# Performance work log

Hardware: AMD Instinct MI355X
Metric: run time of the kernel (lower is better)

The kernel has to match this reference:

```python
import jax, jax.numpy as jnp
import numpy as np

H = 256   # hid_size
N = 10000 # num vertices
B = 512   # num paths
L = 256   # max path length
E = 64    # max neighbors per last vertex


def _init_params(key):
    ks = jax.random.split(key, 12)
    s = 1.0 / np.sqrt(H)
    u = lambda k, shp: jax.random.uniform(k, shp, jnp.float32, -s, s)
    return dict(
        W_ih=u(ks[0], (4 * H, H)), W_hh=u(ks[1], (4 * H, H)),
        b_ih=u(ks[2], (4 * H,)), b_hh=u(ks[3], (4 * H,)),
        Wa1=u(ks[4], (H, 2 * H)), ba1=u(ks[5], (H,)),
        Wa2=u(ks[6], (1, H)), ba2=u(ks[7], (1,)),
        Wc1=u(ks[8], (H, H)), bc1=u(ks[9], (H,)),
        Wc2=u(ks[10], (1, H)), bc2=u(ks[11], (1,)),
    )


def setup_inputs() -> dict:
    key = jax.random.key(0)
    k = jax.random.split(key, 6)
    inp = dict(
        graph_emb=jax.random.normal(k[0], (N, H), jnp.float32),
        paths=jax.random.randint(k[1], (B, L), 0, N),
        path_lens=jax.random.randint(k[2], (B,), 1, L + 1),
        neighbors=jax.random.randint(k[3], (B, E), 0, N),
        n_neighbors=jax.random.randint(k[4], (B,), 1, E + 1),
    )
    inp.update(_init_params(k[5]))
    return inp


def _forward(graph_emb, paths, path_lens, neighbors, n_neighbors,
             W_ih, W_hh, b_ih, b_hh, Wa1, ba1, Wa2, ba2, Wc1, bc1, Wc2, bc2):
    x = graph_emb[paths]  # [B, L, H] gathered path embeddings
    h0 = jnp.zeros((x.shape[0], W_hh.shape[1]), x.dtype)

    def step(carry, inp):
        h, c = carry
        xt, t = inp  # xt: [B, H]
        gates = xt @ W_ih.T + h @ W_hh.T + (b_ih + b_hh)  # [B, 4H], torch gate order i,f,g,o
        i, f, g, o = jnp.split(gates, 4, axis=-1)
        c_new = jax.nn.sigmoid(f) * c + jax.nn.sigmoid(i) * jnp.tanh(g)
        h_new = jax.nn.sigmoid(o) * jnp.tanh(c_new)
        valid = (t < path_lens)[:, None]  # freeze state past each path's length
        return (jnp.where(valid, h_new, h), jnp.where(valid, c_new, c)), None

    (h_final, _), _ = jax.lax.scan(step, (h0, h0),
                                   (x.transpose(1, 0, 2), jnp.arange(x.shape[1])))

    # actor: concat(final hidden, each neighbor emb) -> MLP -> softmax over neighbors
    nb_emb = graph_emb[neighbors]  # [B, E, H]
    states = jnp.concatenate(
        [jnp.broadcast_to(h_final[:, None, :], nb_emb.shape), nb_emb], axis=-1)  # [B, E, 2H]
    a_hid = jax.nn.elu(jnp.einsum('beh,oh->beo', states, Wa1) + ba1)  # [B, E, H]
    logits = (jnp.einsum('beh,oh->beo', a_hid, Wa2) + ba2)[..., 0]    # [B, E]
    mask = jnp.arange(nb_emb.shape[1])[None, :] < n_neighbors[:, None]
    probs = jax.nn.softmax(jnp.where(mask, logits, -1e9), axis=-1)
    probs = probs * mask  # zero out padded neighbor slots

    # critic on the path embedding
    c_hid = jax.nn.elu(h_final @ Wc1.T + bc1)
    values = (c_hid @ Wc2.T + bc2)[:, 0]  # [B]
    return probs, values


def reference(graph_emb, paths, path_lens, neighbors, n_neighbors,
              W_ih, W_hh, b_ih, b_hh, Wa1, ba1, Wa2, ba2, Wc1, bc1, Wc2, bc2):
    return _forward(graph_emb, paths, path_lens, neighbors, n_neighbors,
                    W_ih, W_hh, b_ih, b_hh, Wa1, ba1, Wa2, ba2, Wc1, bc1, Wc2, bc2)
```

## Files before the change

### kernel.cpp

```cpp
#include <hip/hip_runtime.h>
#include <math.h>

#define NV 10000
#define B 512
#define L 256
#define E 64

typedef _Float16 f16;
typedef _Float16 f16x8 __attribute__((ext_vector_type(8)));
typedef float f32x4 __attribute__((ext_vector_type(4)));
typedef int v8i __attribute__((ext_vector_type(8)));

#define OFF_WA1HT 0u
#define OFF_WC1T  65536u
#define OFF_WB    131072u
#define OFF_WIHF  196608u
#define OFF_WA1NF 327680u
#define OFF_PEMB  360448u
#define OFF_AEMB  10600448u

__device__ __forceinline__ int fp8_byte(float x) {
  return __builtin_amdgcn_cvt_pk_fp8_f32(x, x, 0, false) & 0xFF;
}

#define MFMA_SC(a, b, c) \
  __builtin_amdgcn_mfma_scale_f32_16x16x128_f8f6f4((a), (b), (c), 0, 0, 0, 127, 0, 127)

__global__ __launch_bounds__(256) void k_prep(
    const float* __restrict__ W_ih, const float* __restrict__ W_hh,
    const float* __restrict__ Wa1, const float* __restrict__ Wc1,
    float* __restrict__ ws) {
  int idx = blockIdx.x * 256 + threadIdx.x;
  if (idx < 65536) {
    int d = idx & 7, lane = (idx >> 3) & 63, kt = (idx >> 9) & 1;
    int q = (idx >> 10) & 3, w = (idx >> 12) & 15;
    int l15 = lane & 15, quad = lane >> 4;
    int n = q * 256 + w * 16 + l15;
    int kb = kt * 128 + quad * 32 + d * 4;
    unsigned int word = 0;
#pragma unroll
    for (int jb = 0; jb < 4; ++jb)
      word |= ((unsigned int)fp8_byte(W_hh[n * 256 + kb + jb] * 8.f)) << (8 * jb);
    ((unsigned int*)(ws + OFF_WB))[idx] = word;
    return;
  }
  int p1 = idx - 65536;
  if (p1 < 262144) {
    int j = p1 & 7, lane = (p1 >> 3) & 63, kt = (p1 >> 9) & 7;
    int q = (p1 >> 12) & 3, w = (p1 >> 14) & 15;
    int n = q * 256 + w * 16 + (lane & 15);
    int k = kt * 32 + (lane >> 4) * 8 + j;
    ((f16*)(ws + OFF_WIHF))[p1] = (f16)W_ih[n * 256 + k];
    return;
  }
  int p2 = p1 - 262144;
  if (p2 < 65536) {
    int j = p2 & 7, lane = (p2 >> 3) & 63, kt = (p2 >> 9) & 7, w = (p2 >> 12) & 15;
    int n = w * 16 + (lane & 15);
    int k = kt * 32 + (lane >> 4) * 8 + j;
    ((f16*)(ws + OFF_WA1NF))[p2] = (f16)Wa1[n * 512 + 256 + k];
    return;
  }
  int i2 = p2 - 65536;
  if (i2 < 65536) {
    int k = i2 >> 8, j = i2 & 255;
    ws[OFF_WA1HT + i2] = Wa1[j * 512 + k];
    ws[OFF_WC1T + i2] = Wc1[j * 256 + k];
  }
}

__global__ __launch_bounds__(1024) void k_pemb(
    const float* __restrict__ ge, const float* __restrict__ b_ih,
    const float* __restrict__ b_hh, float* __restrict__ ws) {
  __shared__ f16 Alds[32 * 264];
  const int tid = threadIdx.x, w = tid >> 6, lane = tid & 63;
  const int l15 = lane & 15, quad = lane >> 4;
  const int vbase = blockIdx.x * 32;
  for (int i = tid; i < 32 * 256; i += 1024) {
    int row = i >> 8, col = i & 255;
    int v = min(vbase + row, NV - 1);
    Alds[row * 264 + col] = (f16)ge[(size_t)v * 256 + col];
  }
  __syncthreads();
  const f16* __restrict__ WIHF = (const f16*)(ws + OFF_WIHF);
  const f16* __restrict__ WANF = (const f16*)(ws + OFF_WA1NF);
  f32x4 Cp[2][4], Ca[2];
#pragma unroll
  for (int t = 0; t < 2; ++t) {
    Ca[t] = (f32x4){0.f, 0.f, 0.f, 0.f};
#pragma unroll
    for (int q = 0; q < 4; ++q) Cp[t][q] = (f32x4){0.f, 0.f, 0.f, 0.f};
  }
#pragma unroll
  for (int kt = 0; kt < 8; ++kt) {
    f16x8 a0 = *(const f16x8*)(Alds + l15 * 264 + kt * 32 + quad * 8);
    f16x8 a1 = *(const f16x8*)(Alds + (l15 + 16) * 264 + kt * 32 + quad * 8);
#pragma unroll
    for (int q = 0; q < 4; ++q) {
      f16x8 bq = *(const f16x8*)(WIHF + (size_t)(((w * 4 + q) * 8 + kt) * 512 + lane * 8));
      Cp[0][q] = __builtin_amdgcn_mfma_f32_16x16x32_f16(a0, bq, Cp[0][q], 0, 0, 0);
      Cp[1][q] = __builtin_amdgcn_mfma_f32_16x16x32_f16(a1, bq, Cp[1][q], 0, 0, 0);
    }
    f16x8 bn = *(const f16x8*)(WANF + (size_t)((w * 8 + kt) * 512 + lane * 8));
    Ca[0] = __builtin_amdgcn_mfma_f32_16x16x32_f16(a0, bn, Ca[0], 0, 0, 0);
    Ca[1] = __builtin_amdgcn_mfma_f32_16x16x32_f16(a1, bn, Ca[1], 0, 0, 0);
  }
  const int hc = w * 16 + l15;
  float bias[4];
#pragma unroll
  for (int q = 0; q < 4; ++q) {
    int n = q * 256 + hc;
    bias[q] = b_ih[n] + b_hh[n];
  }
  float* __restrict__ P = ws + OFF_PEMB;
  f16* __restrict__ A = (f16*)(ws + OFF_AEMB);
#pragma unroll
  for (int tile = 0; tile < 2; ++tile)
#pragma unroll
    for (int reg = 0; reg < 4; ++reg) {
      int v = vbase + tile * 16 + quad * 4 + reg;
      if (v < NV) {
        f32x4 pw;
#pragma unroll
        for (int q = 0; q < 4; ++q) pw[q] = 128.f * (Cp[tile][q][reg] + bias[q]);
        *(f32x4*)(P + (size_t)v * 1024 + hc * 4) = pw;
        A[(size_t)v * 256 + hc] = (f16)Ca[tile][reg];
      }
    }
}

__global__ __launch_bounds__(1024) void k_lstm(
    const int* __restrict__ paths, const int* __restrict__ path_lens,
    const int* __restrict__ neighbors, const int* __restrict__ n_nb,
    const float* __restrict__ ba1, const float* __restrict__ Wa2,
    const float* __restrict__ ba2, const float* __restrict__ bc1,
    const float* __restrict__ Wc2, const float* __restrict__ bc2,
    float* __restrict__ out, float* __restrict__ ws) {
  const int tid = threadIdx.x, w = tid >> 6, lane = tid & 63;
  const int l15 = lane & 15, quad = lane >> 4;
  const int g2 = blockIdx.x * 2;

  __shared__ char hA[2][4 * 272];
  __shared__ int vtx[2][256];
  __shared__ float hfin[2][257];
  __shared__ float u_s[2][256];
  __shared__ float vred[2][256];
  __shared__ float part8[2][64][8];

  for (int i = tid; i < 2 * 4 * 272 / 4; i += 1024) ((int*)hA)[i] = 0;
  if (tid < 512) vtx[tid >> 8][tid & 255] = paths[(g2 + (tid >> 8)) * L + (tid & 255)];

  const int len0 = path_lens[g2], len1 = path_lens[g2 + 1];
  const int lmax = max(len0, len1);

  const v8i* __restrict__ WBv = (const v8i*)(ws + OFF_WB);
  v8i Bf[4][2];
#pragma unroll
  for (int q = 0; q < 4; ++q)
#pragma unroll
    for (int kt = 0; kt < 2; ++kt)
      Bf[q][kt] = WBv[(size_t)(((w * 4 + q) * 2 + kt) * 64 + lane)];

  const char* __restrict__ Pb = (const char*)(ws + OFF_PEMB);
  const int hc = w * 16 + l15;
  const int path = quad >> 1;
  const int lenv = path ? len1 : len0;
  const unsigned loff = (unsigned)hc * 16u;
  const int physr = ((l15 >> 3) << 1) | (l15 & 1);

  float cst = 0.f, hst = 0.f;
  f32x4 Cf[4];
#pragma unroll
  for (int q = 0; q < 4; ++q) Cf[q] = (f32x4){0.f, 0.f, 0.f, 0.f};
  __syncthreads();

  f32x4 pv = *(const f32x4*)(Pb + (unsigned)vtx[path][0] * 4096u + loff);
  int vn = vtx[path][len0 | len1 ? min(1, L - 1) : 0];

  for (int t = 0; t < lmax; ++t) {
    const char* hp = hA[t & 1];
    const v8i a0 = *(const v8i*)(hp + physr * 272 + quad * 32);
    const v8i a1 = *(const v8i*)(hp + physr * 272 + 128 + quad * 32);
    const int vn2 = vtx[path][min(t + 2, L - 1)];

#pragma unroll
    for (int q = 0; q < 4; ++q) { Cf[q][0] = pv[q]; Cf[q][1] = 0.f; }

    const f32x4 pvn = *(const f32x4*)(Pb + (unsigned)vn * 4096u + loff);

    __builtin_amdgcn_s_setprio(1);
#pragma unroll
    for (int q = 0; q < 4; ++q) Cf[q] = MFMA_SC(a0, Bf[q][0], Cf[q]);
#pragma unroll
    for (int q = 0; q < 4; ++q) Cf[q] = MFMA_SC(a1, Bf[q][1], Cf[q]);
    __builtin_amdgcn_s_setprio(0);

    float G[4];
#pragma unroll
    for (int q = 0; q < 4; ++q) G[q] = Cf[q][0] + Cf[q][1];

    const float inv = 1.f / 128.f;
    const float si = __builtin_amdgcn_rcpf(1.f + __expf(-G[0] * inv));
    const float sf = __builtin_amdgcn_rcpf(1.f + __expf(-G[1] * inv));
    const float tg = 1.f - 2.f * __builtin_amdgcn_rcpf(__expf(2.f * G[2] * inv) + 1.f);
    const float so = __builtin_amdgcn_rcpf(1.f + __expf(-G[3] * inv));
    const float cn = sf * cst + si * tg;
    const float hn = so * (1.f - 2.f * __builtin_amdgcn_rcpf(__expf(2.f * cn) + 1.f));
    if (t < lenv) { cst = cn; hst = hn; }

    if (!(quad & 1)) {
      char* nh = hA[(t + 1) & 1];
      const int hi = fp8_byte(16.f * hst);
      const float d = __builtin_amdgcn_cvt_f32_fp8(hi, 0);
      const int lo = fp8_byte(16.f * hst - d);
      nh[(path * 2 + 0) * 272 + hc] = (char)hi;
      nh[(path * 2 + 1) * 272 + hc] = (char)lo;
    }
    pv = pvn;
    vn = vn2;
    __builtin_amdgcn_sched_barrier(0);
    asm volatile("s_waitcnt lgkmcnt(0)" ::: "memory");
    __builtin_amdgcn_s_barrier();
    __builtin_amdgcn_sched_barrier(0);
  }

  if (!(quad & 1)) hfin[path][hc] = hst;
  __syncthreads();

  const float* __restrict__ Wa1hT = ws + OFF_WA1HT;
  const float* __restrict__ Wc1T = ws + OFF_WC1T;
  const int p = tid >> 9;
  const int jj = tid & 255;
  const int dup = (tid >> 8) & 1;
  if (dup == 0) {
    float aa = ba1[jj];
    for (int k = 0; k < 256; ++k) aa += Wa1hT[k * 256 + jj] * hfin[p][k];
    u_s[p][jj] = aa;
  } else {
    float cc = bc1[jj];
    for (int k = 0; k < 256; ++k) cc += Wc1T[k * 256 + jj] * hfin[p][k];
    cc = cc > 0.f ? cc : __expf(cc) - 1.f;
    vred[p][jj] = cc * Wc2[jj];
  }
  __syncthreads();
  if (tid < 128) {
    const int pp = tid >> 6, lp = tid & 63;
    float s = vred[pp][lp] + vred[pp][lp + 64] + vred[pp][lp + 128] + vred[pp][lp + 192];
#pragma unroll
    for (int d = 32; d > 0; d >>= 1) s += __shfl_xor(s, d, 64);
    if (lp == 0) out[B * E + g2 + pp] = s + bc2[0];
  }
  const f16* __restrict__ A = (const f16*)(ws + OFF_AEMB);
  const int pa = tid >> 9, e = (tid >> 3) & 63, jh = tid & 7;
  const int nbv = neighbors[(g2 + pa) * 64 + e];
  float s = 0.f;
  const f16x8* __restrict__ Arow = (const f16x8*)(A + (size_t)nbv * 256 + jh * 32);
#pragma unroll
  for (int jo = 0; jo < 4; ++jo) {
    const f16x8 av = Arow[jo];
#pragma unroll
    for (int u = 0; u < 8; ++u) {
      const int j = jh * 32 + jo * 8 + u;
      float a = u_s[pa][j] + (float)av[u];
      a = a > 0.f ? a : __expf(a) - 1.f;
      s += a * Wa2[j];
    }
  }
  part8[pa][e][jh] = s;
  __syncthreads();
  if (tid < 128) {
    const int pp = tid >> 6, ee = tid & 63;
    const int ne = n_nb[g2 + pp];
    const bool valid = ee < ne;
    float le = -1e30f;
    if (valid) {
      le = ba2[0];
#pragma unroll
      for (int r = 0; r < 8; ++r) le += part8[pp][ee][r];
    }
    float m = le;
#pragma unroll
    for (int d = 32; d > 0; d >>= 1) m = fmaxf(m, __shfl_xor(m, d, 64));
    float pe = valid ? __expf(le - m) : 0.f;
    float sm = pe;
#pragma unroll
    for (int d = 32; d > 0; d >>= 1) sm += __shfl_xor(sm, d, 64);
    out[(g2 + pp) * 64 + ee] = pe / sm;
  }
}

extern "C" void kernel_launch(void* const* d_in, const int* in_sizes, int n_in,
                              void* d_out, int out_size, void* d_ws, size_t ws_size,
                              hipStream_t stream) {
  (void)in_sizes; (void)n_in; (void)out_size; (void)ws_size;
  const float* graph_emb = (const float*)d_in[0];
  const int* paths       = (const int*)d_in[1];
  const int* path_lens   = (const int*)d_in[2];
  const int* neighbors   = (const int*)d_in[3];
  const int* n_nb        = (const int*)d_in[4];
  const float* W_ih = (const float*)d_in[5];
  const float* W_hh = (const float*)d_in[6];
  const float* b_ih = (const float*)d_in[7];
  const float* b_hh = (const float*)d_in[8];
  const float* Wa1  = (const float*)d_in[9];
  const float* ba1  = (const float*)d_in[10];
  const float* Wa2  = (const float*)d_in[11];
  const float* ba2  = (const float*)d_in[12];
  const float* Wc1  = (const float*)d_in[13];
  const float* bc1  = (const float*)d_in[14];
  const float* Wc2  = (const float*)d_in[15];
  const float* bc2  = (const float*)d_in[16];
  float* out = (float*)d_out;
  float* ws = (float*)d_ws;

  hipLaunchKernelGGL(k_prep, dim3(1792), dim3(256), 0, stream, W_ih, W_hh, Wa1, Wc1, ws);
  hipLaunchKernelGGL(k_pemb, dim3(313), dim3(1024), 0, stream, graph_emb, b_ih, b_hh, ws);
  hipLaunchKernelGGL(k_lstm, dim3(256), dim3(1024), 0, stream, paths, path_lens,
                     neighbors, n_nb, ba1, Wa2, ba2, bc1, Wc2, bc2, out, ws);
}
```

Measured before the change: 350.8 us.

## Halve LSTM block to 512 threads with two hidden columns per lane

The recurrent LSTM kernel now runs with 8 waves instead of 16. Each lane owns two hidden units (hc and hc+128), so it issues 16 MFMAs per step and holds twice the W_hh fragments in registers. The hidden state is written to LDS as packed fp8 pairs, and the k-dimension of W_hh is permuted to match. The goal is cheaper per-step barriers with fewer waves and two blocks per CU, at the cost of more serial work and register pressure per wave on the latency-bound recurrence. The epilogue MLP is also refolded onto 512 threads.

```diff
diff --git a/kernel.cpp b/kernel.cpp
--- a/kernel.cpp
+++ b/kernel.cpp
@@ -22,9 +22,14 @@
 __device__ __forceinline__ int fp8_byte(float x) {
   return __builtin_amdgcn_cvt_pk_fp8_f32(x, x, 0, false) & 0xFF;
 }
+__device__ __forceinline__ unsigned int fp8_pk(float x, float y) {
+  return (unsigned int)__builtin_amdgcn_cvt_pk_fp8_f32(x, y, 0, false);
+}
 
 #define MFMA_SC(a, b, c) \
   __builtin_amdgcn_mfma_scale_f32_16x16x128_f8f6f4((a), (b), (c), 0, 0, 0, 127, 0, 127)
+
+__device__ __forceinline__ int PI(int b) { return ((b & 1) << 7) | (b >> 1); }
 
 __global__ __launch_bounds__(256) void k_prep(
     const float* __restrict__ W_ih, const float* __restrict__ W_hh,
@@ -40,7 +45,7 @@
     unsigned int word = 0;
 #pragma unroll
     for (int jb = 0; jb < 4; ++jb)
-      word |= ((unsigned int)fp8_byte(W_hh[n * 256 + kb + jb] * 8.f)) << (8 * jb);
+      word |= ((unsigned int)fp8_byte(W_hh[n * 256 + PI(kb + jb)] * 8.f)) << (8 * jb);
     ((unsigned int*)(ws + OFF_WB))[idx] = word;
     return;
   }
@@ -129,7 +134,7 @@
     }
 }
 
-__global__ __launch_bounds__(1024) void k_lstm(
+__global__ __launch_bounds__(512, 2) void k_lstm(
     const int* __restrict__ paths, const int* __restrict__ path_lens,
     const int* __restrict__ neighbors, const int* __restrict__ n_nb,
     const float* __restrict__ ba1, const float* __restrict__ Wa2,
@@ -143,23 +148,26 @@
   __shared__ char hA[2][4 * 272];
   __shared__ int vtx[2][256];
   __shared__ float hfin[2][257];
-  __shared__ float u_s[2][256];
-  __shared__ float vred[2][256];
-  __shared__ float part8[2][64][8];
-
-  for (int i = tid; i < 2 * 4 * 272 / 4; i += 1024) ((int*)hA)[i] = 0;
-  if (tid < 512) vtx[tid >> 8][tid & 255] = paths[(g2 + (tid >> 8)) * L + (tid & 255)];
+  __shared__ float u_s[2][264];
+  __shared__ float vredS[2][256];
+  __shared__ float part4[2][64][5];
+
+  for (int i = tid; i < 2 * 4 * 272 / 4; i += 512) ((int*)hA)[i] = 0;
+  vtx[tid >> 8][tid & 255] = paths[(g2 + (tid >> 8)) * L + (tid & 255)];
 
   const int len0 = path_lens[g2], len1 = path_lens[g2 + 1];
   const int lmax = max(len0, len1);
 
   const v8i* __restrict__ WBv = (const v8i*)(ws + OFF_WB);
-  v8i Bf[4][2];
-#pragma unroll
-  for (int q = 0; q < 4; ++q)
+  v8i Bf[8][2];
+#pragma unroll
+  for (int qq = 0; qq < 8; ++qq) {
+    const int wp = (qq < 4) ? w : (w + 8);
+    const int q = qq & 3;
 #pragma unroll
     for (int kt = 0; kt < 2; ++kt)
-      Bf[q][kt] = WBv[(size_t)(((w * 4 + q) * 2 + kt) * 64 + lane)];
+      Bf[qq][kt] = WBv[(size_t)(((wp * 4 + q) * 2 + kt) * 64 + lane)];
+  }
 
   const char* __restrict__ Pb = (const char*)(ws + OFF_PEMB);
   const int hc = w * 16 + l15;
@@ -168,14 +176,15 @@
   const unsigned loff = (unsigned)hc * 16u;
   const int physr = ((l15 >> 3) << 1) | (l15 & 1);
 
-  float cst = 0.f, hst = 0.f;
-  f32x4 Cf[4];
-#pragma unroll
-  for (int q = 0; q < 4; ++q) Cf[q] = (f32x4){0.f, 0.f, 0.f, 0.f};
-  __syncthreads();
-
-  f32x4 pv = *(const f32x4*)(Pb + (unsigned)vtx[path][0] * 4096u + loff);
-  int vn = vtx[path][len0 | len1 ? min(1, L - 1) : 0];
+  float cst0 = 0.f, hst0 = 0.f, cst1 = 0.f, hst1 = 0.f;
+  f32x4 Cf[8];
+#pragma unroll
+  for (int qq = 0; qq < 8; ++qq) Cf[qq] = (f32x4){0.f, 0.f, 0.f, 0.f};
+  __syncthreads();
+
+  f32x4 pva = *(const f32x4*)(Pb + (unsigned)vtx[path][0] * 4096u + loff);
+  f32x4 pvb = *(const f32x4*)(Pb + (unsigned)vtx[path][0] * 4096u + loff + 2048u);
+  int vn = vtx[path][1];
 
   for (int t = 0; t < lmax; ++t) {
     const char* hp = hA[t & 1];
@@ -184,39 +193,59 @@
     const int vn2 = vtx[path][min(t + 2, L - 1)];
 
 #pragma unroll
-    for (int q = 0; q < 4; ++q) { Cf[q][0] = pv[q]; Cf[q][1] = 0.f; }
-
-    const f32x4 pvn = *(const f32x4*)(Pb + (unsigned)vn * 4096u + loff);
+    for (int q = 0; q < 4; ++q) {
+      Cf[q][0] = pva[q];     Cf[q][1] = 0.f;
+      Cf[q + 4][0] = pvb[q]; Cf[q + 4][1] = 0.f;
+    }
+
+    const f32x4 pvna = *(const f32x4*)(Pb + (unsigned)vn * 4096u + loff);
+    const f32x4 pvnb = *(const f32x4*)(Pb + (unsigned)vn * 4096u + loff + 2048u);
 
     __builtin_amdgcn_s_setprio(1);
 #pragma unroll
-    for (int q = 0; q < 4; ++q) Cf[q] = MFMA_SC(a0, Bf[q][0], Cf[q]);
-#pragma unroll
-    for (int q = 0; q < 4; ++q) Cf[q] = MFMA_SC(a1, Bf[q][1], Cf[q]);
+    for (int qq = 0; qq < 8; ++qq) Cf[qq] = MFMA_SC(a0, Bf[qq][0], Cf[qq]);
+#pragma unroll
+    for (int qq = 0; qq < 8; ++qq) Cf[qq] = MFMA_SC(a1, Bf[qq][1], Cf[qq]);
     __builtin_amdgcn_s_setprio(0);
 
-    float G[4];
-#pragma unroll
-    for (int q = 0; q < 4; ++q) G[q] = Cf[q][0] + Cf[q][1];
+    float G0[4], G1[4];
+#pragma unroll
+    for (int q = 0; q < 4; ++q) {
+      G0[q] = Cf[q][0] + Cf[q][1];
+      G1[q] = Cf[q + 4][0] + Cf[q + 4][1];
+    }
 
     const float inv = 1.f / 128.f;
-    const float si = __builtin_amdgcn_rcpf(1.f + __expf(-G[0] * inv));
-    const float sf = __builtin_amdgcn_rcpf(1.f + __expf(-G[1] * inv));
-    const float tg = 1.f - 2.f * __builtin_amdgcn_rcpf(__expf(2.f * G[2] * inv) + 1.f);
-    const float so = __builtin_amdgcn_rcpf(1.f + __expf(-G[3] * inv));
-    const float cn = sf * cst + si * tg;
-    const float hn = so * (1.f - 2.f * __builtin_amdgcn_rcpf(__expf(2.f * cn) + 1.f));
-    if (t < lenv) { cst = cn; hst = hn; }
+    {
+      const float si = __builtin_amdgcn_rcpf(1.f + __expf(-G0[0] * inv));
+      const float sf = __builtin_amdgcn_rcpf(1.f + __expf(-G0[1] * inv));
+      const float tg = 1.f - 2.f * __builtin_amdgcn_rcpf(__expf(2.f * G0[2] * inv) + 1.f);
+      const float so = __builtin_amdgcn_rcpf(1.f + __expf(-G0[3] * inv));
+      const float cn = sf * cst0 + si * tg;
+      const float hn = so * (1.f - 2.f * __builtin_amdgcn_rcpf(__expf(2.f * cn) + 1.f));
+      if (t < lenv) { cst0 = cn; hst0 = hn; }
+    }
+    {
+      const float si = __builtin_amdgcn_rcpf(1.f + __expf(-G1[0] * inv));
+      const float sf = __builtin_amdgcn_rcpf(1.f + __expf(-G1[1] * inv));
+      const float tg = 1.f - 2.f * __builtin_amdgcn_rcpf(__expf(2.f * G1[2] * inv) + 1.f);
+      const float so = __builtin_amdgcn_rcpf(1.f + __expf(-G1[3] * inv));
+      const float cn = sf * cst1 + si * tg;
+      const float hn = so * (1.f - 2.f * __builtin_amdgcn_rcpf(__expf(2.f * cn) + 1.f));
+      if (t < lenv) { cst1 = cn; hst1 = hn; }
+    }
 
     if (!(quad & 1)) {
       char* nh = hA[(t + 1) & 1];
-      const int hi = fp8_byte(16.f * hst);
-      const float d = __builtin_amdgcn_cvt_f32_fp8(hi, 0);
-      const int lo = fp8_byte(16.f * hst - d);
-      nh[(path * 2 + 0) * 272 + hc] = (char)hi;
-      nh[(path * 2 + 1) * 272 + hc] = (char)lo;
-    }
-    pv = pvn;
+      const unsigned int hp2 = fp8_pk(16.f * hst0, 16.f * hst1);
+      const float d0 = __builtin_amdgcn_cvt_f32_fp8((int)hp2, 0);
+      const float d1 = __builtin_amdgcn_cvt_f32_fp8((int)hp2, 1);
+      const unsigned int lp2 = fp8_pk(16.f * hst0 - d0, 16.f * hst1 - d1);
+      *(short*)(nh + (path * 2 + 0) * 272 + 2 * hc) = (short)(hp2 & 0xFFFF);
+      *(short*)(nh + (path * 2 + 1) * 272 + 2 * hc) = (short)(lp2 & 0xFFFF);
+    }
+    pva = pvna;
+    pvb = pvnb;
     vn = vn2;
     __builtin_amdgcn_sched_barrier(0);
     asm volatile("s_waitcnt lgkmcnt(0)" ::: "memory");
@@ -224,49 +253,50 @@
     __builtin_amdgcn_sched_barrier(0);
   }
 
-  if (!(quad & 1)) hfin[path][hc] = hst;
+  if (!(quad & 1)) {
+    hfin[path][hc] = hst0;
+    hfin[path][hc + 128] = hst1;
+  }
   __syncthreads();
 
   const float* __restrict__ Wa1hT = ws + OFF_WA1HT;
   const float* __restrict__ Wc1T = ws + OFF_WC1T;
-  const int p = tid >> 9;
+  const int p = tid >> 8;
   const int jj = tid & 255;
-  const int dup = (tid >> 8) & 1;
-  if (dup == 0) {
-    float aa = ba1[jj];
-    for (int k = 0; k < 256; ++k) aa += Wa1hT[k * 256 + jj] * hfin[p][k];
-    u_s[p][jj] = aa;
-  } else {
-    float cc = bc1[jj];
-    for (int k = 0; k < 256; ++k) cc += Wc1T[k * 256 + jj] * hfin[p][k];
-    cc = cc > 0.f ? cc : __expf(cc) - 1.f;
-    vred[p][jj] = cc * Wc2[jj];
-  }
+  float aa = ba1[jj], cc = bc1[jj];
+  for (int k = 0; k < 256; ++k) {
+    const float hk = hfin[p][k];
+    aa += Wa1hT[k * 256 + jj] * hk;
+    cc += Wc1T[k * 256 + jj] * hk;
+  }
+  u_s[p][jj + (jj >> 5)] = aa;
+  cc = cc > 0.f ? cc : __expf(cc) - 1.f;
+  vredS[p][jj] = cc * Wc2[jj];
   __syncthreads();
   if (tid < 128) {
     const int pp = tid >> 6, lp = tid & 63;
-    float s = vred[pp][lp] + vred[pp][lp + 64] + vred[pp][lp + 128] + vred[pp][lp + 192];
+    float s = vredS[pp][lp] + vredS[pp][lp + 64] + vredS[pp][lp + 128] + vredS[pp][lp + 192];
 #pragma unroll
     for (int d = 32; d > 0; d >>= 1) s += __shfl_xor(s, d, 64);
     if (lp == 0) out[B * E + g2 + pp] = s + bc2[0];
   }
   const f16* __restrict__ A = (const f16*)(ws + OFF_AEMB);
-  const int pa = tid >> 9, e = (tid >> 3) & 63, jh = tid & 7;
+  const int pa = tid >> 8, e = (tid >> 2) & 63, jh = tid & 3;
   const int nbv = neighbors[(g2 + pa) * 64 + e];
   float s = 0.f;
-  const f16x8* __restrict__ Arow = (const f16x8*)(A + (size_t)nbv * 256 + jh * 32);
-#pragma unroll
-  for (int jo = 0; jo < 4; ++jo) {
+  const f16x8* __restrict__ Arow = (const f16x8*)(A + (size_t)nbv * 256 + jh * 64);
+#pragma unroll
+  for (int jo = 0; jo < 8; ++jo) {
     const f16x8 av = Arow[jo];
 #pragma unroll
     for (int u = 0; u < 8; ++u) {
-      const int j = jh * 32 + jo * 8 + u;
-      float a = u_s[pa][j] + (float)av[u];
+      const int j = jh * 64 + jo * 8 + u;
+      float a = u_s[pa][j + (j >> 5)] + (float)av[u];
       a = a > 0.f ? a : __expf(a) - 1.f;
       s += a * Wa2[j];
     }
   }
-  part8[pa][e][jh] = s;
+  part4[pa][e][jh] = s;
   __syncthreads();
   if (tid < 128) {
     const int pp = tid >> 6, ee = tid & 63;
@@ -274,9 +304,7 @@
     const bool valid = ee < ne;
     float le = -1e30f;
     if (valid) {
-      le = ba2[0];
-#pragma unroll
-      for (int r = 0; r < 8; ++r) le += part8[pp][ee][r];
+      le = ba2[0] + part4[pp][ee][0] + part4[pp][ee][1] + part4[pp][ee][2] + part4[pp][ee][3];
     }
     float m = le;
 #pragma unroll
@@ -315,6 +343,6 @@
 
   hipLaunchKernelGGL(k_prep, dim3(1792), dim3(256), 0, stream, W_ih, W_hh, Wa1, Wc1, ws);
   hipLaunchKernelGGL(k_pemb, dim3(313), dim3(1024), 0, stream, graph_emb, b_ih, b_hh, ws);
-  hipLaunchKernelGGL(k_lstm, dim3(256), dim3(1024), 0, stream, paths, path_lens,
+  hipLaunchKernelGGL(k_lstm, dim3(256), dim3(512), 0, stream, paths, path_lens,
                      neighbors, n_nb, ba1, Wa2, ba2, bc1, Wc2, bc2, out, ws);
 }
```

Measured after the change: 373.7 us. 6.5% more time.
